# Optimization experiments

Hardware: AMD Instinct MI355X
Metric: run time of the kernel (lower is better)

## Reference

```python
import jax, jax.numpy as jnp
import numpy as np

MASK_PENALTY = 1e15  # matches the TF module's additive mask constant


def setup_inputs() -> dict:
    key = jax.random.key(0)
    k1, k2, k3, k4, k5 = jax.random.split(key, 5)
    B, S, E, DK, DV = 4, 2048, 1024, 128, 128
    inputs = jax.random.normal(k1, (B, S, E), dtype=jnp.float32)
    mask = jax.random.randint(k2, (B, S, S), 0, 2, dtype=jnp.int32)
    # Dense kernels (glorot-ish scale)
    Wq = jax.random.normal(k3, (E, DK), dtype=jnp.float32) / np.float32(np.sqrt(E))
    Wk = jax.random.normal(k4, (E, DK), dtype=jnp.float32) / np.float32(np.sqrt(E))
    Wv = jax.random.normal(k5, (E, DV), dtype=jnp.float32) / np.float32(np.sqrt(E))
    return {"inputs": inputs, "mask": mask, "Wq": Wq, "Wk": Wk, "Wv": Wv}


def reference(inputs, mask, Wq, Wk, Wv):
    # q, k, v projections (no bias)
    q = jnp.einsum("bse,ed->bsd", inputs, Wq)  # [B,S,DK]
    k = jnp.einsum("bse,ed->bsd", inputs, Wk)  # [B,S,DK]
    v = jnp.einsum("bse,ed->bsd", inputs, Wv)  # [B,S,DV]
    dim_k = Wq.shape[-1]
    scale = jnp.asarray(1.0 / np.sqrt(dim_k), dtype=q.dtype)
    dot_p = jnp.einsum("bqd,bkd->bqk", q, k) * scale  # [B,S,S]
    dot_p = dot_p - MASK_PENALTY * mask.astype(dot_p.dtype)
    softm = jax.nn.softmax(dot_p, axis=-1)
    return jnp.einsum("bqk,bkd->bqd", softm, v)  # [B,S,DV]
```

## Files before the change

kernel.cpp:

```cpp
#include <hip/hip_runtime.h>
#include <stdint.h>


#define SEQ   2048
#define EDIM  1024
#define DDIM  128
#define QSCALE 0.08838834764831845f

typedef unsigned short u16;
typedef unsigned int   u32;
using short8 = __attribute__((ext_vector_type(8))) short;
using f32x4  = __attribute__((ext_vector_type(4))) float;
using int4v  = __attribute__((ext_vector_type(4))) int;

__device__ __forceinline__ u16 f2bf(float x) {
    uint32_t u = __float_as_uint(x);
    return (u16)((u + 0x7fffu + ((u >> 16) & 1u)) >> 16);
}

__device__ __forceinline__ void gld16(const void* gsrc, void* lds_dst) {
    __builtin_amdgcn_global_load_lds(
        (const __attribute__((address_space(1))) uint32_t*)(uintptr_t)gsrc,
        (__attribute__((address_space(3))) uint32_t*)(uint32_t)(uintptr_t)lds_dst,
        16, 0, 0);
}

__global__ __launch_bounds__(256) void prep_kernel(
    const int* __restrict__ mask,
    const float* __restrict__ Wq, const float* __restrict__ Wk, const float* __restrict__ Wv,
    u32* __restrict__ Mbits, u16* __restrict__ Wt)
{
    __shared__ u16 tl[64][65];
    const int bx = blockIdx.x;
    if (bx < 2048) {
        const int word = bx * 256 + threadIdx.x;
        const int* src = mask + (size_t)word * 32;
        u32 bits = 0;
#pragma unroll
        for (int it = 0; it < 8; ++it) {
            const int4v v = *(const int4v*)(src + it * 4);
            bits |= (v[0] != 0 ? 1u : 0u) << (it * 4 + 0);
            bits |= (v[1] != 0 ? 1u : 0u) << (it * 4 + 1);
            bits |= (v[2] != 0 ? 1u : 0u) << (it * 4 + 2);
            bits |= (v[3] != 0 ? 1u : 0u) << (it * 4 + 3);
        }
        Mbits[word] = bits;
    } else {
        const int t = bx - 2048;
        const int wsel = t >> 5;
        const int tile = t & 31;
        const int k0 = (tile >> 1) * 64;
        const int n0 = (tile & 1) * 64;
        const float* W = (wsel == 0) ? Wq : ((wsel == 1) ? Wk : Wv);
#pragma unroll
        for (int it = 0; it < 16; ++it) {
            const int idx = it * 256 + threadIdx.x;
            const int r = idx >> 6, c = idx & 63;
            tl[c][r] = f2bf(W[(size_t)(k0 + r) * DDIM + n0 + c]);
        }
        __syncthreads();
        u16* Wtp = Wt + (size_t)wsel * DDIM * EDIM;
#pragma unroll
        for (int it = 0; it < 16; ++it) {
            const int idx = it * 256 + threadIdx.x;
            const int r = idx >> 6, c = idx & 63;
            Wtp[(size_t)(n0 + r) * EDIM + k0 + c] = tl[r][c];
        }
    }
}

__global__ __launch_bounds__(256, 2) void proj_kernel(
    const float* __restrict__ Ain, const u16* __restrict__ Wtb,
    u16* __restrict__ Qb, u16* __restrict__ Kb, u16* __restrict__ Vtb)
{
    __shared__ __align__(16) uint8_t smem[32768];
    const int tid = threadIdx.x;
    const int w = tid >> 6, lane = tid & 63;
    const int lq = lane & 15, lg = lane >> 4;
    const int wr = w >> 1, wc = w & 1;

    const int bid = blockIdx.x;
    const int wg = (bid & 7) * 24 + (bid >> 3);
    const int wm = wg % 3;
    const int m0 = (wg / 3) * 128;
    const u16* Wt = Wtb + (size_t)wm * DDIM * EDIM;

    f32x4 acc[4][4] = {};

#pragma unroll 1
    for (int kt = 0; kt < 16; ++kt) {
        const int k0 = kt * 64;
#pragma unroll
        for (int i = 0; i < 4; ++i) {
            const int G = i * 256 + tid;
            const int n = G >> 3, c = G & 7;
            gld16(Wt + (size_t)n * EDIM + k0 + ((c ^ (n & 7)) << 3),
                  smem + 16384 + i * 4096 + w * 1024);
        }
#pragma unroll
        for (int i = 0; i < 4; ++i) {
            const int G = i * 256 + tid;
            const int row = G >> 3, c = G & 7;
            const float* s2 = Ain + (size_t)(m0 + row) * EDIM + k0 + ((c ^ (row & 7)) << 3);
            const f32x4 a0 = *(const f32x4*)s2;
            const f32x4 a1 = *(const f32x4*)(s2 + 4);
            short8 v;
            v[0] = (short)f2bf(a0[0]); v[1] = (short)f2bf(a0[1]);
            v[2] = (short)f2bf(a0[2]); v[3] = (short)f2bf(a0[3]);
            v[4] = (short)f2bf(a1[0]); v[5] = (short)f2bf(a1[1]);
            v[6] = (short)f2bf(a1[2]); v[7] = (short)f2bf(a1[3]);
            *(short8*)(smem + row * 128 + (c << 4)) = v;
        }
        __syncthreads();
#pragma unroll
        for (int ks = 0; ks < 2; ++ks) {
            short8 af[4], bfv[4];
#pragma unroll
            for (int mf = 0; mf < 4; ++mf) {
                const int arow = wr * 64 + mf * 16 + lq;
                af[mf] = *(const short8*)(smem + arow * 128 + ((((ks << 2) + lg) ^ (arow & 7)) << 4));
            }
#pragma unroll
            for (int nf = 0; nf < 4; ++nf) {
                const int brow = wc * 64 + nf * 16 + lq;
                bfv[nf] = *(const short8*)(smem + 16384 + brow * 128 + ((((ks << 2) + lg) ^ (brow & 7)) << 4));
            }
#pragma unroll
            for (int mf = 0; mf < 4; ++mf)
#pragma unroll
                for (int nf = 0; nf < 4; ++nf)
                    acc[mf][nf] = __builtin_amdgcn_mfma_f32_16x16x32_bf16(af[mf], bfv[nf], acc[mf][nf], 0, 0, 0);
        }
        __syncthreads();
    }

    const float osc = (wm == 0) ? QSCALE : 1.0f;
    if (wm < 2) {
#pragma unroll
        for (int mf = 0; mf < 4; ++mf)
#pragma unroll
            for (int nf = 0; nf < 4; ++nf)
#pragma unroll
                for (int rr = 0; rr < 4; ++rr) {
                    const int row = wr * 64 + mf * 16 + lg * 4 + rr;
                    const int col = wc * 64 + nf * 16 + lq;
                    *(u16*)(smem + row * 256 + (((col >> 3) ^ (row & 7)) << 4) + ((col & 7) << 1))
                        = f2bf(acc[mf][nf][rr] * osc);
                }
        __syncthreads();
        u16* dst = (wm == 0 ? Qb : Kb) + (size_t)m0 * 128;
#pragma unroll
        for (int i = 0; i < 8; ++i) {
            const int j = i * 256 + tid;
            const int row = j >> 4, c = j & 15;
            *(short8*)(dst + (size_t)row * 128 + c * 8)
                = *(const short8*)(smem + row * 256 + ((c ^ (row & 7)) << 4));
        }
    } else {
#pragma unroll
        for (int mf = 0; mf < 4; ++mf)
#pragma unroll
            for (int nf = 0; nf < 4; ++nf)
#pragma unroll
                for (int rr = 0; rr < 4; ++rr) {
                    const int sl = wr * 64 + mf * 16 + lg * 4 + rr;
                    const int d  = wc * 64 + nf * 16 + lq;
                    *(u16*)(smem + d * 256 + (((sl >> 3) ^ (d & 7)) << 4) + ((sl & 7) << 1))
                        = f2bf(acc[mf][nf][rr]);
                }
        __syncthreads();
        const int b = m0 >> 11, s0b = m0 & 2047;
        u16* dst = Vtb + (size_t)b * DDIM * SEQ;
#pragma unroll
        for (int i = 0; i < 8; ++i) {
            const int j = i * 256 + tid;
            const int dd = j >> 4, c = j & 15;
            *(short8*)(dst + (size_t)dd * SEQ + s0b + c * 8)
                = *(const short8*)(smem + dd * 256 + ((c ^ (dd & 7)) << 4));
        }
    }
}

__global__ __launch_bounds__(256, 2) void flash_kernel(
    const u32* __restrict__ Mb,
    const u16* __restrict__ Qb, const u16* __restrict__ Kb, const u16* __restrict__ Vtb,
    float* __restrict__ out)
{
    __shared__ __align__(16) uint8_t smem[69632];
    __shared__ float ml_m[4][16], ml_l[4][16], recipL[16];

    const int tid = threadIdx.x;
    const int w = tid >> 6, lane = tid & 63;
    const int lq = lane & 15, lg = lane >> 4;

    const int bid = blockIdx.x;
    const int qt = (bid & 7) * 64 + (bid >> 3);
    const int b = qt >> 7;
    const int q0 = (qt & 127) << 4;
    const size_t qrow0 = (size_t)b * SEQ + q0;

    const u16* Qp = Qb + qrow0 * 128;
    const u16* Kp = Kb + (size_t)b * SEQ * 128;
    const u16* Vp = Vtb + (size_t)b * DDIM * SEQ;

    short8 qf[4];
#pragma unroll
    for (int ks = 0; ks < 4; ++ks)
        qf[ks] = *(const short8*)(Qp + (size_t)lq * 128 + ks * 32 + lg * 8);

    f32x4 acc[8] = {};
    float mrow[4], lrow[4];
#pragma unroll
    for (int r = 0; r < 4; ++r) { mrow[r] = -1e30f; lrow[r] = 0.0f; }

    uint8_t* kvbase = smem + w * 16384;

#pragma unroll 1
    for (int t = 0; t < 16; ++t) {
        const int kv0 = w * 512 + t * 32;
        const int kvw = w * 16 + t;
        asm volatile("s_waitcnt lgkmcnt(0)" ::: "memory");
        __builtin_amdgcn_sched_barrier(0);
#pragma unroll
        for (int i = 0; i < 8; ++i) {
            const int G = i * 64 + lane;
            const int row = G >> 4, c = G & 15;
            gld16(Kp + (size_t)(kv0 + row) * 128 + (c ^ (row & 7)) * 8,
                  kvbase + i * 1024);
        }
        __builtin_amdgcn_sched_barrier(0);
        u32 mw[4];
#pragma unroll
        for (int r = 0; r < 4; ++r)
            mw[r] = Mb[(qrow0 + lg * 4 + r) * 64 + kvw];
        __builtin_amdgcn_sched_barrier(0);
#pragma unroll
        for (int i = 0; i < 8; ++i) {
            const int G = i * 64 + lane;
            const int dd = G >> 2, c = G & 3;
            gld16(Vp + (size_t)dd * SEQ + kv0 + (c ^ ((dd ^ (dd >> 2)) & 3)) * 8,
                  kvbase + 8192 + i * 1024);
        }
        __builtin_amdgcn_sched_barrier(0);
        asm volatile("s_waitcnt vmcnt(8)" ::: "memory");

        f32x4 sacc[2] = {};
#pragma unroll
        for (int ks = 0; ks < 4; ++ks) {
#pragma unroll
            for (int nf = 0; nf < 2; ++nf) {
                const int krow = nf * 16 + lq;
                const short8 kf = *(const short8*)(kvbase + krow * 256 + ((((ks << 2) + lg) ^ (krow & 7)) << 4));
                sacc[nf] = __builtin_amdgcn_mfma_f32_16x16x32_bf16(qf[ks], kf, sacc[nf], 0, 0, 0);
            }
        }

        float sv[2][4], tm[4];
#pragma unroll
        for (int r = 0; r < 4; ++r) {
            sv[0][r] = sacc[0][r] + (((mw[r] >> lq) & 1u)        ? -1e15f : 0.0f);
            sv[1][r] = sacc[1][r] + (((mw[r] >> (16 + lq)) & 1u) ? -1e15f : 0.0f);
        }
#pragma unroll
        for (int r = 0; r < 4; ++r) tm[r] = fmaxf(sv[0][r], sv[1][r]);
#pragma unroll
        for (int d = 1; d < 16; d <<= 1)
#pragma unroll
            for (int r = 0; r < 4; ++r)
                tm[r] = fmaxf(tm[r], __shfl_xor(tm[r], d));

        float sf[4];
#pragma unroll
        for (int r = 0; r < 4; ++r) {
            const float mnew = fmaxf(mrow[r], tm[r]);
            sf[r] = __expf(mrow[r] - mnew);
            mrow[r] = mnew;
        }
        float p[2][4], rs[4];
#pragma unroll
        for (int nf = 0; nf < 2; ++nf)
#pragma unroll
            for (int r = 0; r < 4; ++r)
                p[nf][r] = __expf(sv[nf][r] - mrow[r]);
#pragma unroll
        for (int r = 0; r < 4; ++r) rs[r] = p[0][r] + p[1][r];
#pragma unroll
        for (int d = 1; d < 16; d <<= 1)
#pragma unroll
            for (int r = 0; r < 4; ++r)
                rs[r] += __shfl_xor(rs[r], d);
#pragma unroll
        for (int r = 0; r < 4; ++r) lrow[r] = lrow[r] * sf[r] + rs[r];
#pragma unroll
        for (int df = 0; df < 8; ++df)
#pragma unroll
            for (int r = 0; r < 4; ++r)
                acc[df][r] *= sf[r];

        uint8_t* pbase = smem + 65536 + w * 1024;
#pragma unroll
        for (int nf = 0; nf < 2; ++nf)
#pragma unroll
            for (int r = 0; r < 4; ++r) {
                const int row = lg * 4 + r, col = nf * 16 + lq;
                *(u16*)(pbase + row * 64 + ((((col >> 3) ^ ((row ^ (row >> 2)) & 3))) << 4) + (col & 7) * 2)
                    = f2bf(p[nf][r]);
            }
        const short8 pf = *(const short8*)(pbase + lq * 64 + ((lg ^ ((lq ^ (lq >> 2)) & 3)) << 4));
        asm volatile("s_waitcnt vmcnt(0)" ::: "memory");
        __builtin_amdgcn_sched_barrier(0);
#pragma unroll
        for (int nf = 0; nf < 8; ++nf) {
            const int dd = nf * 16 + lq;
            const short8 vf = *(const short8*)(kvbase + 8192 + dd * 64 + ((lg ^ ((dd ^ (dd >> 2)) & 3)) << 4));
            acc[nf] = __builtin_amdgcn_mfma_f32_16x16x32_bf16(pf, vf, acc[nf], 0, 0, 0);
        }
    }

    if (lq == 0) {
#pragma unroll
        for (int r = 0; r < 4; ++r) {
            ml_m[w][lg * 4 + r] = mrow[r];
            ml_l[w][lg * 4 + r] = lrow[r];
        }
    }
    __syncthreads();
    float Lg[4];
#pragma unroll
    for (int r = 0; r < 4; ++r) {
        const int row = lg * 4 + r;
        const float m0v = ml_m[0][row], m1v = ml_m[1][row], m2v = ml_m[2][row], m3v = ml_m[3][row];
        const float mm = fmaxf(fmaxf(m0v, m1v), fmaxf(m2v, m3v));
        Lg[r] = ml_l[0][row] * __expf(m0v - mm) + ml_l[1][row] * __expf(m1v - mm)
              + ml_l[2][row] * __expf(m2v - mm) + ml_l[3][row] * __expf(m3v - mm);
        const float s = __expf(mrow[r] - mm);
#pragma unroll
        for (int df = 0; df < 8; ++df) acc[df][r] *= s;
    }
    if (w == 0 && lq == 0) {
#pragma unroll
        for (int r = 0; r < 4; ++r) recipL[lg * 4 + r] = 1.0f / Lg[r];
    }
    float* Ol = (float*)smem;
#pragma unroll
    for (int df = 0; df < 8; ++df)
#pragma unroll
        for (int r = 0; r < 4; ++r)
            Ol[(size_t)(w * 16 + lg * 4 + r) * 128 + df * 16 + lq] = acc[df][r];
    __syncthreads();

    {
        const int idx = tid * 8;
        const int row = idx >> 7, c0 = idx & 127;
        const float rl = recipL[row];
        f32x4 s0 = {}, s1 = {};
#pragma unroll
        for (int wv = 0; wv < 4; ++wv) {
            const float* p2 = Ol + (size_t)(wv * 16 + row) * 128 + c0;
            s0 += *(const f32x4*)p2;
            s1 += *(const f32x4*)(p2 + 4);
        }
        s0 *= rl; s1 *= rl;
        float* op = out + (qrow0 + row) * 128 + c0;
        *(f32x4*)op = s0;
        *(f32x4*)(op + 4) = s1;
    }
}

extern "C" void kernel_launch(void* const* d_in, const int* in_sizes, int n_in,
                              void* d_out, int out_size, void* d_ws, size_t ws_size,
                              hipStream_t stream) {
    (void)in_sizes; (void)n_in; (void)out_size; (void)ws_size;
    const float* inputs = (const float*)d_in[0];
    const int*   mask   = (const int*)d_in[1];
    const float* Wq     = (const float*)d_in[2];
    const float* Wk     = (const float*)d_in[3];
    const float* Wv     = (const float*)d_in[4];
    float* out = (float*)d_out;

    uint8_t* ws = (uint8_t*)d_ws;
    u16* Wtb   = (u16*)ws;
    u16* Qb    = (u16*)(ws + 786432);
    u16* Kb    = (u16*)(ws + 2883584);
    u16* Vtb   = (u16*)(ws + 4980736);
    u32* Mbits = (u32*)(ws + 7077888);

    hipLaunchKernelGGL(prep_kernel, dim3(2144), dim3(256), 0, stream, mask, Wq, Wk, Wv, Mbits, Wtb);
    hipLaunchKernelGGL(proj_kernel, dim3(192), dim3(256), 0, stream, inputs, Wtb, Qb, Kb, Vtb);
    hipLaunchKernelGGL(flash_kernel, dim3(512), dim3(256), 0, stream, Mbits, Qb, Kb, Vtb, out);
}
```

Baseline: 188.4 us.

## Rework mask packing, shrink projection tiles, register-prefetch K/V in flash kernel

The mask packer now reads the int mask fully coalesced per block and assembles 32-bit words through a swizzled LDS nibble buffer. The projection kernel moves from 128-row to 32-row tiles, going from 192 to 768 blocks at a higher occupancy target. The flash kernel drops LDS staging of K/V and loads MFMA fragments straight from global memory into registers with one-tile prefetch. It also uses transposed MFMA operands, so each lane owns one query row and the row max/sum reductions need fewer shuffles. The trade-off is more register pressure and uncached global fragment loads against less LDS traffic and better parallelism.

```diff
diff --git a/kernel.cpp b/kernel.cpp
--- a/kernel.cpp
+++ b/kernel.cpp
@@ -30,21 +30,26 @@
     const float* __restrict__ Wq, const float* __restrict__ Wk, const float* __restrict__ Wv,
     u32* __restrict__ Mbits, u16* __restrict__ Wt)
 {
+    __shared__ u32 nib32[2048];
     __shared__ u16 tl[64][65];
     const int bx = blockIdx.x;
+    const int tid = threadIdx.x;
     if (bx < 2048) {
-        const int word = bx * 256 + threadIdx.x;
-        const int* src = mask + (size_t)word * 32;
-        u32 bits = 0;
+        const int* src = mask + (size_t)bx * 8192;
 #pragma unroll
         for (int it = 0; it < 8; ++it) {
-            const int4v v = *(const int4v*)(src + it * 4);
-            bits |= (v[0] != 0 ? 1u : 0u) << (it * 4 + 0);
-            bits |= (v[1] != 0 ? 1u : 0u) << (it * 4 + 1);
-            bits |= (v[2] != 0 ? 1u : 0u) << (it * 4 + 2);
-            bits |= (v[3] != 0 ? 1u : 0u) << (it * 4 + 3);
-        }
-        Mbits[word] = bits;
+            const int idx = it * 256 + tid;
+            const int4v v = *(const int4v*)(src + idx * 4);
+            const u32 nb = (v[0] != 0 ? 1u : 0u) | (v[1] != 0 ? 2u : 0u)
+                         | (v[2] != 0 ? 4u : 0u) | (v[3] != 0 ? 8u : 0u);
+            nib32[(idx & 7) * 256 + ((idx >> 3) ^ ((idx & 7) << 2))] = nb;
+        }
+        __syncthreads();
+        u32 word = 0;
+#pragma unroll
+        for (int j = 0; j < 8; ++j)
+            word |= (nib32[j * 256 + (tid ^ (j << 2))] & 0xFu) << (4 * j);
+        Mbits[bx * 256 + tid] = word;
     } else {
         const int t = bx - 2048;
         const int wsel = t >> 5;
@@ -54,7 +59,7 @@
         const float* W = (wsel == 0) ? Wq : ((wsel == 1) ? Wk : Wv);
 #pragma unroll
         for (int it = 0; it < 16; ++it) {
-            const int idx = it * 256 + threadIdx.x;
+            const int idx = it * 256 + tid;
             const int r = idx >> 6, c = idx & 63;
             tl[c][r] = f2bf(W[(size_t)(k0 + r) * DDIM + n0 + c]);
         }
@@ -62,30 +67,29 @@
         u16* Wtp = Wt + (size_t)wsel * DDIM * EDIM;
 #pragma unroll
         for (int it = 0; it < 16; ++it) {
-            const int idx = it * 256 + threadIdx.x;
+            const int idx = it * 256 + tid;
             const int r = idx >> 6, c = idx & 63;
             Wtp[(size_t)(n0 + r) * EDIM + k0 + c] = tl[r][c];
         }
     }
 }
 
-__global__ __launch_bounds__(256, 2) void proj_kernel(
+__global__ __launch_bounds__(256, 3) void proj_kernel(
     const float* __restrict__ Ain, const u16* __restrict__ Wtb,
     u16* __restrict__ Qb, u16* __restrict__ Kb, u16* __restrict__ Vtb)
 {
-    __shared__ __align__(16) uint8_t smem[32768];
+    __shared__ __align__(16) uint8_t smem[20480];
     const int tid = threadIdx.x;
     const int w = tid >> 6, lane = tid & 63;
     const int lq = lane & 15, lg = lane >> 4;
-    const int wr = w >> 1, wc = w & 1;
 
     const int bid = blockIdx.x;
-    const int wg = (bid & 7) * 24 + (bid >> 3);
+    const int wg = (bid & 7) * 96 + (bid >> 3);
     const int wm = wg % 3;
-    const int m0 = (wg / 3) * 128;
+    const int m0 = (wg / 3) * 32;
     const u16* Wt = Wtb + (size_t)wm * DDIM * EDIM;
 
-    f32x4 acc[4][4] = {};
+    f32x4 acc[2][2] = {};
 
 #pragma unroll 1
     for (int kt = 0; kt < 16; ++kt) {
@@ -95,12 +99,10 @@
             const int G = i * 256 + tid;
             const int n = G >> 3, c = G & 7;
             gld16(Wt + (size_t)n * EDIM + k0 + ((c ^ (n & 7)) << 3),
-                  smem + 16384 + i * 4096 + w * 1024);
-        }
-#pragma unroll
-        for (int i = 0; i < 4; ++i) {
-            const int G = i * 256 + tid;
-            const int row = G >> 3, c = G & 7;
+                  smem + 4096 + i * 4096 + w * 1024);
+        }
+        {
+            const int row = tid >> 3, c = tid & 7;
             const float* s2 = Ain + (size_t)(m0 + row) * EDIM + k0 + ((c ^ (row & 7)) << 3);
             const f32x4 a0 = *(const f32x4*)s2;
             const f32x4 a1 = *(const f32x4*)(s2 + 4);
@@ -114,21 +116,21 @@
         __syncthreads();
 #pragma unroll
         for (int ks = 0; ks < 2; ++ks) {
-            short8 af[4], bfv[4];
-#pragma unroll
-            for (int mf = 0; mf < 4; ++mf) {
-                const int arow = wr * 64 + mf * 16 + lq;
+            short8 af[2], bfv[2];
+#pragma unroll
+            for (int mf = 0; mf < 2; ++mf) {
+                const int arow = mf * 16 + lq;
                 af[mf] = *(const short8*)(smem + arow * 128 + ((((ks << 2) + lg) ^ (arow & 7)) << 4));
             }
 #pragma unroll
-            for (int nf = 0; nf < 4; ++nf) {
-                const int brow = wc * 64 + nf * 16 + lq;
-                bfv[nf] = *(const short8*)(smem + 16384 + brow * 128 + ((((ks << 2) + lg) ^ (brow & 7)) << 4));
+            for (int nf = 0; nf < 2; ++nf) {
+                const int brow = w * 32 + nf * 16 + lq;
+                bfv[nf] = *(const short8*)(smem + 4096 + brow * 128 + ((((ks << 2) + lg) ^ (brow & 7)) << 4));
             }
 #pragma unroll
-            for (int mf = 0; mf < 4; ++mf)
-#pragma unroll
-                for (int nf = 0; nf < 4; ++nf)
+            for (int mf = 0; mf < 2; ++mf)
+#pragma unroll
+                for (int nf = 0; nf < 2; ++nf)
                     acc[mf][nf] = __builtin_amdgcn_mfma_f32_16x16x32_bf16(af[mf], bfv[nf], acc[mf][nf], 0, 0, 0);
         }
         __syncthreads();
@@ -137,20 +139,20 @@
     const float osc = (wm == 0) ? QSCALE : 1.0f;
     if (wm < 2) {
 #pragma unroll
-        for (int mf = 0; mf < 4; ++mf)
-#pragma unroll
-            for (int nf = 0; nf < 4; ++nf)
+        for (int mf = 0; mf < 2; ++mf)
+#pragma unroll
+            for (int nf = 0; nf < 2; ++nf)
 #pragma unroll
                 for (int rr = 0; rr < 4; ++rr) {
-                    const int row = wr * 64 + mf * 16 + lg * 4 + rr;
-                    const int col = wc * 64 + nf * 16 + lq;
+                    const int row = mf * 16 + lg * 4 + rr;
+                    const int col = w * 32 + nf * 16 + lq;
                     *(u16*)(smem + row * 256 + (((col >> 3) ^ (row & 7)) << 4) + ((col & 7) << 1))
                         = f2bf(acc[mf][nf][rr] * osc);
                 }
         __syncthreads();
         u16* dst = (wm == 0 ? Qb : Kb) + (size_t)m0 * 128;
 #pragma unroll
-        for (int i = 0; i < 8; ++i) {
+        for (int i = 0; i < 2; ++i) {
             const int j = i * 256 + tid;
             const int row = j >> 4, c = j & 15;
             *(short8*)(dst + (size_t)row * 128 + c * 8)
@@ -158,25 +160,25 @@
         }
     } else {
 #pragma unroll
-        for (int mf = 0; mf < 4; ++mf)
-#pragma unroll
-            for (int nf = 0; nf < 4; ++nf)
+        for (int mf = 0; mf < 2; ++mf)
+#pragma unroll
+            for (int nf = 0; nf < 2; ++nf)
 #pragma unroll
                 for (int rr = 0; rr < 4; ++rr) {
-                    const int sl = wr * 64 + mf * 16 + lg * 4 + rr;
-                    const int d  = wc * 64 + nf * 16 + lq;
-                    *(u16*)(smem + d * 256 + (((sl >> 3) ^ (d & 7)) << 4) + ((sl & 7) << 1))
+                    const int sl = mf * 16 + lg * 4 + rr;
+                    const int d  = w * 32 + nf * 16 + lq;
+                    *(u16*)(smem + d * 64 + (((sl >> 3) ^ (d & 3)) << 4) + ((sl & 7) << 1))
                         = f2bf(acc[mf][nf][rr]);
                 }
         __syncthreads();
         const int b = m0 >> 11, s0b = m0 & 2047;
         u16* dst = Vtb + (size_t)b * DDIM * SEQ;
 #pragma unroll
-        for (int i = 0; i < 8; ++i) {
+        for (int i = 0; i < 2; ++i) {
             const int j = i * 256 + tid;
-            const int dd = j >> 4, c = j & 15;
+            const int dd = j >> 2, c = j & 3;
             *(short8*)(dst + (size_t)dd * SEQ + s0b + c * 8)
-                = *(const short8*)(smem + dd * 256 + ((c ^ (dd & 7)) << 4));
+                = *(const short8*)(smem + dd * 64 + ((c ^ (dd & 3)) << 4));
         }
     }
 }
@@ -186,7 +188,7 @@
     const u16* __restrict__ Qb, const u16* __restrict__ Kb, const u16* __restrict__ Vtb,
     float* __restrict__ out)
 {
-    __shared__ __align__(16) uint8_t smem[69632];
+    __shared__ __align__(16) uint8_t smem[36864];
     __shared__ float ml_m[4][16], ml_l[4][16], recipL[16];
 
     const int tid = threadIdx.x;
@@ -202,6 +204,7 @@
     const u16* Qp = Qb + qrow0 * 128;
     const u16* Kp = Kb + (size_t)b * SEQ * 128;
     const u16* Vp = Vtb + (size_t)b * DDIM * SEQ;
+    const u32* mrp = Mb + (qrow0 + lq) * 64 + w * 16;
 
     short8 qf[4];
 #pragma unroll
@@ -209,149 +212,108 @@
         qf[ks] = *(const short8*)(Qp + (size_t)lq * 128 + ks * 32 + lg * 8);
 
     f32x4 acc[8] = {};
-    float mrow[4], lrow[4];
-#pragma unroll
-    for (int r = 0; r < 4; ++r) { mrow[r] = -1e30f; lrow[r] = 0.0f; }
-
-    uint8_t* kvbase = smem + w * 16384;
+    float m = -1e30f, l = 0.0f;
+
+    const int kv00 = w * 512;
+    short8 kf[2][4], vf[8];
+    u32 mw;
+#pragma unroll
+    for (int nf = 0; nf < 2; ++nf)
+#pragma unroll
+        for (int ks = 0; ks < 4; ++ks)
+            kf[nf][ks] = *(const short8*)(Kp + (size_t)(kv00 + nf * 16 + lq) * 128 + ks * 32 + lg * 8);
+#pragma unroll
+    for (int df = 0; df < 8; ++df)
+        vf[df] = *(const short8*)(Vp + (size_t)(df * 16 + lq) * SEQ + kv00 + lg * 8);
+    mw = mrp[0];
+
+    uint8_t* pbase = smem + 32768 + w * 1024;
 
 #pragma unroll 1
     for (int t = 0; t < 16; ++t) {
-        const int kv0 = w * 512 + t * 32;
-        const int kvw = w * 16 + t;
-        asm volatile("s_waitcnt lgkmcnt(0)" ::: "memory");
-        __builtin_amdgcn_sched_barrier(0);
-#pragma unroll
-        for (int i = 0; i < 8; ++i) {
-            const int G = i * 64 + lane;
-            const int row = G >> 4, c = G & 15;
-            gld16(Kp + (size_t)(kv0 + row) * 128 + (c ^ (row & 7)) * 8,
-                  kvbase + i * 1024);
-        }
-        __builtin_amdgcn_sched_barrier(0);
-        u32 mw[4];
-#pragma unroll
-        for (int r = 0; r < 4; ++r)
-            mw[r] = Mb[(qrow0 + lg * 4 + r) * 64 + kvw];
-        __builtin_amdgcn_sched_barrier(0);
-#pragma unroll
-        for (int i = 0; i < 8; ++i) {
-            const int G = i * 64 + lane;
-            const int dd = G >> 2, c = G & 3;
-            gld16(Vp + (size_t)dd * SEQ + kv0 + (c ^ ((dd ^ (dd >> 2)) & 3)) * 8,
-                  kvbase + 8192 + i * 1024);
-        }
-        __builtin_amdgcn_sched_barrier(0);
-        asm volatile("s_waitcnt vmcnt(8)" ::: "memory");
-
+        const int tn = (t < 15) ? t + 1 : 15;
+        const int kvn = kv00 + tn * 32;
+        __builtin_amdgcn_sched_barrier(0);
         f32x4 sacc[2] = {};
 #pragma unroll
-        for (int ks = 0; ks < 4; ++ks) {
-#pragma unroll
-            for (int nf = 0; nf < 2; ++nf) {
-                const int krow = nf * 16 + lq;
-                const short8 kf = *(const short8*)(kvbase + krow * 256 + ((((ks << 2) + lg) ^ (krow & 7)) << 4));
-                sacc[nf] = __builtin_amdgcn_mfma_f32_16x16x32_bf16(qf[ks], kf, sacc[nf], 0, 0, 0);
+        for (int ks = 0; ks < 4; ++ks)
+#pragma unroll
+            for (int nf = 0; nf < 2; ++nf)
+                sacc[nf] = __builtin_amdgcn_mfma_f32_16x16x32_bf16(kf[nf][ks], qf[ks], sacc[nf], 0, 0, 0);
+        __builtin_amdgcn_sched_barrier(0);
+#pragma unroll
+        for (int nf = 0; nf < 2; ++nf)
+#pragma unroll
+            for (int ks = 0; ks < 4; ++ks)
+                kf[nf][ks] = *(const short8*)(Kp + (size_t)(kvn + nf * 16 + lq) * 128 + ks * 32 + lg * 8);
+        __builtin_amdgcn_sched_barrier(0);
+        float sv[2][4];
+#pragma unroll
+        for (int nf = 0; nf < 2; ++nf)
+#pragma unroll
+            for (int r = 0; r < 4; ++r)
+                sv[nf][r] = sacc[nf][r] + (((mw >> (nf * 16 + lg * 4 + r)) & 1u) ? -1e15f : 0.0f);
+        float tm = sv[0][0];
+#pragma unroll
+        for (int nf = 0; nf < 2; ++nf)
+#pragma unroll
+            for (int r = 0; r < 4; ++r) tm = fmaxf(tm, sv[nf][r]);
+        tm = fmaxf(tm, __shfl_xor(tm, 16));
+        tm = fmaxf(tm, __shfl_xor(tm, 32));
+        const float mnew = fmaxf(m, tm);
+        const float sf = __expf(m - mnew);
+        m = mnew;
+        float p[2][4];
+        float rs = 0.0f;
+#pragma unroll
+        for (int nf = 0; nf < 2; ++nf)
+#pragma unroll
+            for (int r = 0; r < 4; ++r) { p[nf][r] = __expf(sv[nf][r] - m); rs += p[nf][r]; }
+        rs += __shfl_xor(rs, 16);
+        rs += __shfl_xor(rs, 32);
+        l = l * sf + rs;
+        mw = mrp[tn];
+#pragma unroll
+        for (int df = 0; df < 8; ++df) acc[df] *= sf;
+#pragma unroll
+        for (int nf = 0; nf < 2; ++nf)
+#pragma unroll
+            for (int h = 0; h < 2; ++h) {
+                const u32 pk = (u32)f2bf(p[nf][2 * h]) | ((u32)f2bf(p[nf][2 * h + 1]) << 16);
+                const int kv = lg * 4 + 2 * h + 16 * nf;
+                *(u32*)(pbase + lq * 64 + (((kv >> 3) ^ (lq & 3)) << 4) + ((kv << 1) & 15)) = pk;
             }
-        }
-
-        float sv[2][4], tm[4];
-#pragma unroll
-        for (int r = 0; r < 4; ++r) {
-            sv[0][r] = sacc[0][r] + (((mw[r] >> lq) & 1u)        ? -1e15f : 0.0f);
-            sv[1][r] = sacc[1][r] + (((mw[r] >> (16 + lq)) & 1u) ? -1e15f : 0.0f);
-        }
-#pragma unroll
-        for (int r = 0; r < 4; ++r) tm[r] = fmaxf(sv[0][r], sv[1][r]);
-#pragma unroll
-        for (int d = 1; d < 16; d <<= 1)
-#pragma unroll
-            for (int r = 0; r < 4; ++r)
-                tm[r] = fmaxf(tm[r], __shfl_xor(tm[r], d));
-
-        float sf[4];
-#pragma unroll
-        for (int r = 0; r < 4; ++r) {
-            const float mnew = fmaxf(mrow[r], tm[r]);
-            sf[r] = __expf(mrow[r] - mnew);
-            mrow[r] = mnew;
-        }
-        float p[2][4], rs[4];
-#pragma unroll
-        for (int nf = 0; nf < 2; ++nf)
-#pragma unroll
-            for (int r = 0; r < 4; ++r)
-                p[nf][r] = __expf(sv[nf][r] - mrow[r]);
-#pragma unroll
-        for (int r = 0; r < 4; ++r) rs[r] = p[0][r] + p[1][r];
-#pragma unroll
-        for (int d = 1; d < 16; d <<= 1)
-#pragma unroll
-            for (int r = 0; r < 4; ++r)
-                rs[r] += __shfl_xor(rs[r], d);
-#pragma unroll
-        for (int r = 0; r < 4; ++r) lrow[r] = lrow[r] * sf[r] + rs[r];
+        const short8 pf = *(const short8*)(pbase + lq * 64 + ((lg ^ (lq & 3)) << 4));
+        __builtin_amdgcn_sched_barrier(0);
 #pragma unroll
         for (int df = 0; df < 8; ++df)
-#pragma unroll
-            for (int r = 0; r < 4; ++r)
-                acc[df][r] *= sf[r];
-
-        uint8_t* pbase = smem + 65536 + w * 1024;
-#pragma unroll
-        for (int nf = 0; nf < 2; ++nf)
-#pragma unroll
-            for (int r = 0; r < 4; ++r) {
-                const int row = lg * 4 + r, col = nf * 16 + lq;
-                *(u16*)(pbase + row * 64 + ((((col >> 3) ^ ((row ^ (row >> 2)) & 3))) << 4) + (col & 7) * 2)
-                    = f2bf(p[nf][r]);
-            }
-        const short8 pf = *(const short8*)(pbase + lq * 64 + ((lg ^ ((lq ^ (lq >> 2)) & 3)) << 4));
-        asm volatile("s_waitcnt vmcnt(0)" ::: "memory");
-        __builtin_amdgcn_sched_barrier(0);
-#pragma unroll
-        for (int nf = 0; nf < 8; ++nf) {
-            const int dd = nf * 16 + lq;
-            const short8 vf = *(const short8*)(kvbase + 8192 + dd * 64 + ((lg ^ ((dd ^ (dd >> 2)) & 3)) << 4));
-            acc[nf] = __builtin_amdgcn_mfma_f32_16x16x32_bf16(pf, vf, acc[nf], 0, 0, 0);
-        }
-    }
-
-    if (lq == 0) {
-#pragma unroll
-        for (int r = 0; r < 4; ++r) {
-            ml_m[w][lg * 4 + r] = mrow[r];
-            ml_l[w][lg * 4 + r] = lrow[r];
-        }
-    }
+            acc[df] = __builtin_amdgcn_mfma_f32_16x16x32_bf16(vf[df], pf, acc[df], 0, 0, 0);
+        __builtin_amdgcn_sched_barrier(0);
+#pragma unroll
+        for (int df = 0; df < 8; ++df)
+            vf[df] = *(const short8*)(Vp + (size_t)(df * 16 + lq) * SEQ + kvn + lg * 8);
+    }
+
+    if (lg == 0) { ml_m[w][lq] = m; ml_l[w][lq] = l; }
     __syncthreads();
-    float Lg[4];
-#pragma unroll
-    for (int r = 0; r < 4; ++r) {
-        const int row = lg * 4 + r;
-        const float m0v = ml_m[0][row], m1v = ml_m[1][row], m2v = ml_m[2][row], m3v = ml_m[3][row];
+    {
+        const float m0v = ml_m[0][lq], m1v = ml_m[1][lq], m2v = ml_m[2][lq], m3v = ml_m[3][lq];
         const float mm = fmaxf(fmaxf(m0v, m1v), fmaxf(m2v, m3v));
-        Lg[r] = ml_l[0][row] * __expf(m0v - mm) + ml_l[1][row] * __expf(m1v - mm)
-              + ml_l[2][row] * __expf(m2v - mm) + ml_l[3][row] * __expf(m3v - mm);
-        const float s = __expf(mrow[r] - mm);
-#pragma unroll
-        for (int df = 0; df < 8; ++df) acc[df][r] *= s;
-    }
-    if (w == 0 && lq == 0) {
-#pragma unroll
-        for (int r = 0; r < 4; ++r) recipL[lg * 4 + r] = 1.0f / Lg[r];
-    }
-    float* Ol = (float*)smem;
-#pragma unroll
-    for (int df = 0; df < 8; ++df)
-#pragma unroll
-        for (int r = 0; r < 4; ++r)
-            Ol[(size_t)(w * 16 + lg * 4 + r) * 128 + df * 16 + lq] = acc[df][r];
+        const float Lg = ml_l[0][lq] * __expf(m0v - mm) + ml_l[1][lq] * __expf(m1v - mm)
+                       + ml_l[2][lq] * __expf(m2v - mm) + ml_l[3][lq] * __expf(m3v - mm);
+        const float s = __expf(m - mm);
+        if (w == 0 && lg == 0) recipL[lq] = 1.0f / Lg;
+        float* Ol = (float*)smem;
+#pragma unroll
+        for (int df = 0; df < 8; ++df) {
+            const f32x4 vsc = acc[df] * s;
+            *(f32x4*)(Ol + (size_t)(w * 16 + lq) * 128 + df * 16 + lg * 4) = vsc;
+        }
+    }
     __syncthreads();
-
     {
-        const int idx = tid * 8;
-        const int row = idx >> 7, c0 = idx & 127;
+        const float* Ol = (const float*)smem;
+        const int row = tid >> 4, c0 = (tid & 15) * 8;
         const float rl = recipL[row];
         f32x4 s0 = {}, s1 = {};
 #pragma unroll
@@ -386,6 +348,6 @@
     u32* Mbits = (u32*)(ws + 7077888);
 
     hipLaunchKernelGGL(prep_kernel, dim3(2144), dim3(256), 0, stream, mask, Wq, Wk, Wv, Mbits, Wtb);
-    hipLaunchKernelGGL(proj_kernel, dim3(192), dim3(256), 0, stream, inputs, Wtb, Qb, Kb, Vtb);
+    hipLaunchKernelGGL(proj_kernel, dim3(768), dim3(256), 0, stream, inputs, Wtb, Qb, Kb, Vtb);
     hipLaunchKernelGGL(flash_kernel, dim3(512), dim3(256), 0, stream, Mbits, Qb, Kb, Vtb, out);
 }
```

After: 202.9 us. +7.7%, slower.
